# Kernel optimization log

Measured on AMD Instinct MI355X. Metric: run time of the kernel, lower is better.

Reference implementation:

```python
import jax, jax.numpy as jnp
import numpy as np

B, T, D, H = 2, 2048, 1024, 16
HD = D // H


def setup_inputs() -> dict:
    key = jax.random.key(0)
    ks = jax.random.split(key, 9)
    s = 1.0 / np.sqrt(D)
    return {
        "x": jax.random.normal(ks[0], (B, T, D), dtype=jnp.float32),
        "Wq": jax.random.normal(ks[1], (D, D), dtype=jnp.float32) * s,
        "bq": jnp.zeros((D,), dtype=jnp.float32),
        "Wk": jax.random.normal(ks[2], (D, D), dtype=jnp.float32) * s,
        "bk": jnp.zeros((D,), dtype=jnp.float32),
        "Wv": jax.random.normal(ks[3], (D, D), dtype=jnp.float32) * s,
        "bv": jnp.zeros((D,), dtype=jnp.float32),
        "Wo": jax.random.normal(ks[4], (D, D), dtype=jnp.float32) * s,
        "bo": jnp.zeros((D,), dtype=jnp.float32),
    }


def reference(x, Wq, bq, Wk, bk, Wv, bv, Wo, bo):
    b, t, d = x.shape
    # projections, split heads: (b, h, t, hd)
    def heads(y):
        return y.reshape(b, t, H, HD).transpose(0, 2, 1, 3)
    Q = heads(x @ Wq + bq)
    K = heads(x @ Wk + bk)
    V = heads(x @ Wv + bv)
    # scores scaled by sqrt(d) (full embed dim, faithful to source)
    score = jnp.einsum("bhid,bhjd->bhij", Q, K) / jnp.sqrt(jnp.float32(d))
    causal = jnp.triu(jnp.ones((t, t), dtype=bool), k=1)  # (t, t)
    score = jnp.where(causal, jnp.float32(-1e10), score)
    # FAITHFUL quirk: softmax over the HEAD axis (torch dim=1 of [b,h,t,t])
    weight = jax.nn.softmax(score, axis=1)
    out = jnp.einsum("bhij,bhjd->bhid", weight, V)
    out = out.transpose(0, 2, 1, 3).reshape(b, t, d)
    return out @ Wo + bo
```

## Files before the change

### kernel.cpp

```cpp
#include <hip/hip_runtime.h>
#include <hip/hip_bf16.h>

#define B_ 2
#define T_ 2048
#define D_ 1024
#define H_ 16

typedef __attribute__((ext_vector_type(8))) short bf16x8;
typedef __attribute__((ext_vector_type(4))) short bf16x4;
typedef __attribute__((ext_vector_type(4))) float f32x4;

__device__ __forceinline__ unsigned pack_bf16(float x, float y) {
  unsigned xb = __float_as_uint(x), yb = __float_as_uint(y);
  xb += 0x7fffu + ((xb >> 16) & 1u);
  yb += 0x7fffu + ((yb >> 16) & 1u);
  return (xb >> 16) | (yb & 0xffff0000u);
}
__device__ __forceinline__ unsigned short f2b(float x) {
  unsigned u = __float_as_uint(x);
  u += 0x7fffu + ((u >> 16) & 1u);
  return (unsigned short)(u >> 16);
}
__device__ __forceinline__ float blo(unsigned u) { return __uint_as_float(u << 16); }
__device__ __forceinline__ float bhi(unsigned u) { return __uint_as_float(u & 0xffff0000u); }

__device__ __forceinline__ void gld_lds16(const unsigned short* g, unsigned short* l) {
  __builtin_amdgcn_global_load_lds(
      (const __attribute__((address_space(1))) unsigned int*)g,
      (__attribute__((address_space(3))) unsigned int*)l, 16, 0, 0);
}

__global__ __launch_bounds__(256) void wtrans(const float* __restrict__ W0, const float* __restrict__ W1,
                                              const float* __restrict__ W2, const float* __restrict__ W3,
                                              unsigned short* __restrict__ T0, unsigned short* __restrict__ T1,
                                              unsigned short* __restrict__ T2, unsigned short* __restrict__ T3) {
  const int z = blockIdx.z;
  const float* W = z == 0 ? W0 : z == 1 ? W1 : z == 2 ? W2 : W3;
  unsigned short* T = z == 0 ? T0 : z == 1 ? T1 : z == 2 ? T2 : T3;
  __shared__ unsigned short t[64][72];
  const int k0 = blockIdx.x << 6, n0 = blockIdx.y << 6;
  const int r = threadIdx.x >> 2, c16 = (threadIdx.x & 3) << 4;
#pragma unroll
  for (int e = 0; e < 4; ++e) {
    const float4 v = *(const float4*)&W[(size_t)(k0 + r) * 1024 + n0 + c16 + e * 4];
    t[r][c16 + e * 4 + 0] = f2b(v.x);
    t[r][c16 + e * 4 + 1] = f2b(v.y);
    t[r][c16 + e * 4 + 2] = f2b(v.z);
    t[r][c16 + e * 4 + 3] = f2b(v.w);
  }
  __syncthreads();
  unsigned short o[16];
#pragma unroll
  for (int e = 0; e < 16; ++e) o[e] = t[c16 + e][r];
  unsigned short* dst = &T[(size_t)(n0 + r) * 1024 + k0 + c16];
  *(uint4*)&dst[0] = *(uint4*)&o[0];
  *(uint4*)&dst[8] = *(uint4*)&o[8];
}

__global__ __launch_bounds__(256) void xconv(const float* __restrict__ x, unsigned short* __restrict__ xb) {
  const int i = (blockIdx.x * 256 + threadIdx.x) * 8;
  const float4 a = *(const float4*)&x[i];
  const float4 b = *(const float4*)&x[i + 4];
  uint4 o;
  o.x = pack_bf16(a.x, a.y);
  o.y = pack_bf16(a.z, a.w);
  o.z = pack_bf16(b.x, b.y);
  o.w = pack_bf16(b.z, b.w);
  *(uint4*)&xb[i] = o;
}

template <bool BF16OUT>
__global__ __launch_bounds__(256) void gemm_mfma(const unsigned short* __restrict__ A,
                                                 const unsigned short* __restrict__ B0,
                                                 const unsigned short* __restrict__ B1,
                                                 const unsigned short* __restrict__ B2,
                                                 const float* __restrict__ bi0, const float* __restrict__ bi1,
                                                 const float* __restrict__ bi2,
                                                 void* __restrict__ Y0, void* __restrict__ Y1,
                                                 void* __restrict__ Y2) {
  const int z = blockIdx.z;
  const unsigned short* Bt = z == 0 ? B0 : z == 1 ? B1 : B2;
  const float* bias = z == 0 ? bi0 : z == 1 ? bi1 : bi2;
  void* Y = z == 0 ? Y0 : z == 1 ? Y1 : Y2;
  __shared__ unsigned short As[8192];
  __shared__ unsigned short Bs[8192];
  const int tid = threadIdx.x;
  const int m0 = blockIdx.y << 7, n0 = blockIdx.x << 7;
  const int w = tid >> 6, l = tid & 63, g = l >> 4, c = l & 15;
  const int wm = (w >> 1) << 6, wn = (w & 1) << 6;
  const int srow = tid >> 3;
  const int skel = ((tid & 7) ^ (srow & 7)) << 3;
  const unsigned short* ga = &A[(size_t)(m0 + srow) * 1024 + skel];
  const unsigned short* gb = &Bt[(size_t)(n0 + srow) * 1024 + skel];
  unsigned short* la = &As[tid << 3];
  unsigned short* lb = &Bs[tid << 3];
  f32x4 acc[4][4];
#pragma unroll
  for (int i = 0; i < 4; ++i)
#pragma unroll
    for (int j = 0; j < 4; ++j) acc[i][j] = {0.f, 0.f, 0.f, 0.f};
  for (int k0 = 0; k0 < 1024; k0 += 64) {
    __syncthreads();
#pragma unroll
    for (int a = 0; a < 4; ++a) {
      gld_lds16(ga + (size_t)(a << 5) * 1024 + k0, la + (a << 11));
      gld_lds16(gb + (size_t)(a << 5) * 1024 + k0, lb + (a << 11));
    }
    __syncthreads();
#pragma unroll
    for (int kc = 0; kc < 2; ++kc) {
      bf16x8 af[4], bfr[4];
#pragma unroll
      for (int mf = 0; mf < 4; ++mf) {
        const int m = wm + (mf << 4) + c;
        af[mf] = *(const bf16x8*)&As[((m << 6) + (kc << 5) + (g << 3)) ^ ((m & 7) << 3)];
      }
#pragma unroll
      for (int nf = 0; nf < 4; ++nf) {
        const int n = wn + (nf << 4) + c;
        bfr[nf] = *(const bf16x8*)&Bs[((n << 6) + (kc << 5) + (g << 3)) ^ ((n & 7) << 3)];
      }
#pragma unroll
      for (int mf = 0; mf < 4; ++mf)
#pragma unroll
        for (int nf = 0; nf < 4; ++nf)
          acc[mf][nf] = __builtin_amdgcn_mfma_f32_16x16x32_bf16(af[mf], bfr[nf], acc[mf][nf], 0, 0, 0);
    }
  }
#pragma unroll
  for (int nf = 0; nf < 4; ++nf) {
    const int n = n0 + wn + (nf << 4) + c;
    const float bb = bias[n];
#pragma unroll
    for (int mf = 0; mf < 4; ++mf) {
      const int mrow = m0 + wm + (mf << 4) + (g << 2);
#pragma unroll
      for (int r = 0; r < 4; ++r) {
        const float val = acc[mf][nf][r] + bb;
        if (BF16OUT)
          ((unsigned short*)Y)[((size_t)(mrow + r) << 10) + n] = f2b(val);
        else
          ((float*)Y)[((size_t)(mrow + r) << 10) + n] = val;
      }
    }
  }
}

__global__ __launch_bounds__(256) void transpose_bf16(const unsigned short* __restrict__ Vb,
                                                      unsigned short* __restrict__ Vt) {
  __shared__ unsigned short tile[64][73];
  const int b = blockIdx.z;
  const int t0 = blockIdx.x << 6, d0 = blockIdx.y << 6;
  const int row = threadIdx.x >> 2, cq = (threadIdx.x & 3) << 4;
  const unsigned short* src = &Vb[((size_t)((b << 11) + t0 + row) << 10) + d0 + cq];
  const uint4 va = *(const uint4*)&src[0];
  const uint4 vb2 = *(const uint4*)&src[8];
  const unsigned in[8] = {va.x, va.y, va.z, va.w, vb2.x, vb2.y, vb2.z, vb2.w};
#pragma unroll
  for (int e = 0; e < 8; ++e) {
    tile[row][cq + 2 * e] = (unsigned short)in[e];
    tile[row][cq + 2 * e + 1] = (unsigned short)(in[e] >> 16);
  }
  __syncthreads();
  unsigned o[8];
#pragma unroll
  for (int e = 0; e < 8; ++e)
    o[e] = (unsigned)tile[cq + 2 * e][row] | ((unsigned)tile[cq + 2 * e + 1][row] << 16);
  unsigned short* dst = &Vt[((size_t)((b << 10) + d0 + row) << 11) + t0 + cq];
  uint4 lo, hi;
  lo.x = o[0]; lo.y = o[1]; lo.z = o[2]; lo.w = o[3];
  hi.x = o[4]; hi.y = o[5]; hi.z = o[6]; hi.w = o[7];
  *(uint4*)&dst[0] = lo;
  *(uint4*)&dst[8] = hi;
}

__global__ __launch_bounds__(256) void vblk32(const unsigned short* __restrict__ Vb,
                                              float* __restrict__ Blk) {
  const int b = blockIdx.x >> 6, t = blockIdx.x & 63;
  const int d4 = threadIdx.x << 2;
  float s0 = 0.f, s1 = 0.f, s2 = 0.f, s3 = 0.f;
  for (int j = 0; j < 32; ++j) {
    const uint2 v = *(const uint2*)&Vb[((size_t)((b << 11) + (t << 5) + j) << 10) + d4];
    s0 += blo(v.x); s1 += bhi(v.x); s2 += blo(v.y); s3 += bhi(v.y);
  }
  float4 o = {s0, s1, s2, s3};
  *(float4*)&Blk[((size_t)((b << 6) + t) << 10) + d4] = o;
}

__global__ __launch_bounds__(256) void vsuffix32(const float* __restrict__ Blk, float* __restrict__ Suf) {
  const int idx = blockIdx.x * 256 + threadIdx.x;
  const int b = idx >> 10, d = idx & 1023;
  float s = 0.f;
  Suf[((size_t)(b * 65 + 64) << 10) + d] = 0.f;
  for (int t = 63; t >= 0; --t) {
    s += Blk[((size_t)((b << 6) + t) << 10) + d];
    Suf[((size_t)(b * 65 + t) << 10) + d] = s;
  }
}

__global__ __launch_bounds__(1024, 4) void attn_v16(const unsigned short* __restrict__ Qb,
                                                    const unsigned short* __restrict__ Kb,
                                                    const unsigned short* __restrict__ Vt,
                                                    unsigned short* __restrict__ P0,
                                                    unsigned short* __restrict__ P1,
                                                    unsigned short* __restrict__ P2,
                                                    unsigned short* __restrict__ P3) {
  __shared__ unsigned short Ks[2][16 * 1024];
  __shared__ unsigned short Vs[2][1024 * 16];
  __shared__ f32x4 Sx[2][8][64];

  const int combo = blockIdx.x;
  const int b = combo & 1, s = combo >> 1;
  const int qy = 63 - blockIdx.y;
  const int tid = threadIdx.x;
  const int w = tid >> 6, l = tid & 63, g = l >> 4, c = l & 15;
  const int isub = w >> 3, hp = w & 7;
  const float SC = 0.04508422f;
  unsigned short* AOp = s == 0 ? P0 : s == 1 ? P1 : s == 2 ? P2 : P3;

  const int krow0 = tid >> 7, kc8 = tid & 127;
  const int kscc = kc8 ^ (krow0 & 7);
  const int krow1 = (tid + 1024) >> 7, kc8b = tid & 127;
  const int ksccb = kc8b ^ (krow1 & 7);

#pragma unroll
  for (int ph = 0; ph < 2; ++ph) {
    const int q = ph ? (63 - qy) : qy;
    const int nt16 = (q + 1) << 1;
    const int i0w = (q << 5) + (isub << 4);
    const int ib = i0w + c;

    const unsigned short* qbase =
        &Qb[((size_t)((b << 11) + i0w + c) << 10) + (hp << 7) + (g << 3)];
    bf16x8 qf[4];
    qf[0] = *(const bf16x8*)&qbase[0];
    qf[1] = *(const bf16x8*)&qbase[32];
    qf[2] = *(const bf16x8*)&qbase[64];
    qf[3] = *(const bf16x8*)&qbase[96];

    f32x4 acc[2][4];
#pragma unroll
    for (int hh = 0; hh < 2; ++hh)
#pragma unroll
      for (int cc = 0; cc < 4; ++cc) acc[hh][cc] = {0.f, 0.f, 0.f, 0.f};

#pragma unroll
    for (int e = 0; e < 2; ++e) {
      const int eh = e ? (7 - s) : s;
      const int lo = eh << 4;
      const int hi = (lo + 16) < nt16 ? (lo + 16) : nt16;
      if (lo >= hi) continue;

      {
        const int j0e = lo << 4;
        gld_lds16(&Kb[((size_t)((b << 11) + j0e + krow0) << 10) + (kscc << 3)], &Ks[0][tid << 3]);
        gld_lds16(&Kb[((size_t)((b << 11) + j0e + krow1) << 10) + (ksccb << 3)],
                  &Ks[0][(tid + 1024) << 3]);
#pragma unroll
        for (int kk = 0; kk < 2; ++kk) {
          const int qq = tid + (kk << 10);
          const int d = qq >> 1, jc = qq & 1;
          const int joff = ((jc << 1) ^ (((d >> 2) & 1) << 1)) << 2;
          gld_lds16(&Vt[(((size_t)((b << 10) + d)) << 11) + j0e + joff], &Vs[0][qq << 3]);
        }
      }
      __syncthreads();

      for (int ts = lo; ts < hi; ++ts) {
        const int cur = (ts - lo) & 1;
        if (ts + 1 < hi) {
          const int j0e = (ts + 1) << 4;
          gld_lds16(&Kb[((size_t)((b << 11) + j0e + krow0) << 10) + (kscc << 3)],
                    &Ks[cur ^ 1][tid << 3]);
          gld_lds16(&Kb[((size_t)((b << 11) + j0e + krow1) << 10) + (ksccb << 3)],
                    &Ks[cur ^ 1][(tid + 1024) << 3]);
#pragma unroll
          for (int kk = 0; kk < 2; ++kk) {
            const int qq = tid + (kk << 10);
            const int d = qq >> 1, jc = qq & 1;
            const int joff = ((jc << 1) ^ (((d >> 2) & 1) << 1)) << 2;
            gld_lds16(&Vt[(((size_t)((b << 10) + d)) << 11) + j0e + joff],
                      &Vs[cur ^ 1][qq << 3]);
          }
        }
        const int j0 = ts << 4;
        const int kx = c & 7;
        f32x4 ex[2];
        f32x4 ps = {0.f, 0.f, 0.f, 0.f};
#pragma unroll
        for (int hh = 0; hh < 2; ++hh) {
          const int hc = ((hp << 1) + hh) << 3;
          const bf16x8 k0 = *(const bf16x8*)&Ks[cur][((c << 7) + ((hc + g) ^ kx)) << 3];
          const bf16x8 k1 = *(const bf16x8*)&Ks[cur][((c << 7) + ((hc + 4 + g) ^ kx)) << 3];
          f32x4 a = {0.f, 0.f, 0.f, 0.f};
          a = __builtin_amdgcn_mfma_f32_16x16x32_bf16(k0, qf[2 * hh], a, 0, 0, 0);
          a = __builtin_amdgcn_mfma_f32_16x16x32_bf16(k1, qf[2 * hh + 1], a, 0, 0, 0);
#pragma unroll
          for (int r = 0; r < 4; ++r) ex[hh][r] = exp2f(a[r] * SC);
          ps += ex[hh];
        }
        Sx[isub][hp][l] = ps;
        __syncthreads();
        f32x4 sum = Sx[isub][0][l];
#pragma unroll
        for (int d8 = 1; d8 < 8; ++d8) sum += Sx[isub][d8][l];
        f32x4 inv;
#pragma unroll
        for (int r = 0; r < 4; ++r) inv[r] = __builtin_amdgcn_rcpf(sum[r]);
        float wv[2][4];
        if (j0 + 15 <= i0w) {
#pragma unroll
          for (int hh = 0; hh < 2; ++hh)
#pragma unroll
            for (int r = 0; r < 4; ++r) wv[hh][r] = ex[hh][r] * inv[r];
        } else {
          const int jb = j0 + (g << 2);
#pragma unroll
          for (int hh = 0; hh < 2; ++hh)
#pragma unroll
            for (int r = 0; r < 4; ++r)
              wv[hh][r] = (jb + r > ib) ? 0.0625f : ex[hh][r] * inv[r];
        }
#pragma unroll
        for (int hh = 0; hh < 2; ++hh) {
          union { bf16x4 v; unsigned u[2]; } pa;
          pa.u[0] = pack_bf16(wv[hh][0], wv[hh][1]);
          pa.u[1] = pack_bf16(wv[hh][2], wv[hh][3]);
#pragma unroll
          for (int cc = 0; cc < 4; ++cc) {
            const int d = (((hp << 1) + hh) << 6) + (cc << 4) + c;
            const int up = g ^ (((d >> 2) & 1) << 1);
            union { bf16x4 v; unsigned u[2]; } vf;
            *(uint2*)&vf = *(const uint2*)&Vs[cur][(d << 4) + (up << 2)];
            acc[hh][cc] =
                __builtin_amdgcn_mfma_f32_16x16x16bf16_1k(pa.v, vf.v, acc[hh][cc], 0, 0, 0);
          }
        }
        __syncthreads();
      }
    }
#pragma unroll
    for (int hh = 0; hh < 2; ++hh)
#pragma unroll
      for (int cc = 0; cc < 4; ++cc) {
        const int d = (((hp << 1) + hh) << 6) + (cc << 4) + c;
#pragma unroll
        for (int r = 0; r < 4; ++r)
          AOp[((size_t)((b << 11) + i0w + (g << 2) + r) << 10) + d] = f2b(acc[hh][cc][r]);
      }
  }
}

__global__ __launch_bounds__(256) void aocvt(const unsigned short* __restrict__ P0,
                                             const unsigned short* __restrict__ P1,
                                             const unsigned short* __restrict__ P2,
                                             const unsigned short* __restrict__ P3,
                                             const float* __restrict__ Suf,
                                             unsigned short* __restrict__ AOb) {
  const int i = (blockIdx.x * 256 + threadIdx.x) << 3;
  const int m = i >> 10;
  const int b = m >> 11;
  const int sufidx = ((m & 2047) >> 5) + 1;
  const int d0 = i & 1023;
  const float* sp = &Suf[((size_t)(b * 65 + sufidx) << 10) + d0];
  const uint4 v0 = *(const uint4*)&P0[i];
  const uint4 v1 = *(const uint4*)&P1[i];
  const uint4 v2 = *(const uint4*)&P2[i];
  const uint4 v3 = *(const uint4*)&P3[i];
  const float4 s0 = *(const float4*)&sp[0];
  const float4 s1 = *(const float4*)&sp[4];
  uint4 o;
  o.x = pack_bf16(blo(v0.x) + blo(v1.x) + blo(v2.x) + blo(v3.x) + 0.0625f * s0.x,
                  bhi(v0.x) + bhi(v1.x) + bhi(v2.x) + bhi(v3.x) + 0.0625f * s0.y);
  o.y = pack_bf16(blo(v0.y) + blo(v1.y) + blo(v2.y) + blo(v3.y) + 0.0625f * s0.z,
                  bhi(v0.y) + bhi(v1.y) + bhi(v2.y) + bhi(v3.y) + 0.0625f * s0.w);
  o.z = pack_bf16(blo(v0.z) + blo(v1.z) + blo(v2.z) + blo(v3.z) + 0.0625f * s1.x,
                  bhi(v0.z) + bhi(v1.z) + bhi(v2.z) + bhi(v3.z) + 0.0625f * s1.y);
  o.w = pack_bf16(blo(v0.w) + blo(v1.w) + blo(v2.w) + blo(v3.w) + 0.0625f * s1.z,
                  bhi(v0.w) + bhi(v1.w) + bhi(v2.w) + bhi(v3.w) + 0.0625f * s1.w);
  *(uint4*)&AOb[i] = o;
}

extern "C" void kernel_launch(void* const* d_in, const int* in_sizes, int n_in,
                              void* d_out, int out_size, void* d_ws, size_t ws_size,
                              hipStream_t stream) {
  (void)in_sizes; (void)n_in; (void)out_size; (void)ws_size;
  const float* x = (const float*)d_in[0];
  const float* Wq = (const float*)d_in[1];
  const float* bq = (const float*)d_in[2];
  const float* Wk = (const float*)d_in[3];
  const float* bk = (const float*)d_in[4];
  const float* Wv = (const float*)d_in[5];
  const float* bv = (const float*)d_in[6];
  const float* Wo = (const float*)d_in[7];
  const float* bo = (const float*)d_in[8];
  float* out = (float*)d_out;
  char* ws = (char*)d_ws;

  const size_t MB = 1024 * 1024;
  unsigned short* xb  = (unsigned short*)(ws);
  unsigned short* Qb  = (unsigned short*)(ws + 8 * MB);
  unsigned short* Kb  = (unsigned short*)(ws + 16 * MB);
  unsigned short* Vb  = (unsigned short*)(ws + 24 * MB);
  unsigned short* Vt  = (unsigned short*)(ws + 32 * MB);
  unsigned short* Wqt = (unsigned short*)(ws + 40 * MB);
  unsigned short* Wkt = (unsigned short*)(ws + 42 * MB);
  unsigned short* Wvt = (unsigned short*)(ws + 44 * MB);
  unsigned short* Wot = (unsigned short*)(ws + 46 * MB);
  unsigned short* AOP2 = (unsigned short*)(ws + 48 * MB);
  unsigned short* AOP3 = (unsigned short*)(ws + 56 * MB);
  float* Blk = (float*)(ws + 40 * MB);
  float* Suf = (float*)(ws + 40 * MB + 512 * 1024);
  unsigned short* AOP0 = xb;
  unsigned short* AOP1 = Vb;
  unsigned short* AOb = Qb;

  hipLaunchKernelGGL(wtrans, dim3(16, 16, 4), dim3(256), 0, stream,
                     Wq, Wk, Wv, Wo, Wqt, Wkt, Wvt, Wot);
  hipLaunchKernelGGL(xconv, dim3(2048), dim3(256), 0, stream, x, xb);
  hipLaunchKernelGGL((gemm_mfma<true>), dim3(8, 32, 3), dim3(256), 0, stream,
                     xb, Wqt, Wkt, Wvt, bq, bk, bv, (void*)Qb, (void*)Kb, (void*)Vb);
  hipLaunchKernelGGL(transpose_bf16, dim3(32, 16, 2), dim3(256), 0, stream, Vb, Vt);
  hipLaunchKernelGGL(vblk32, dim3(128), dim3(256), 0, stream, Vb, Blk);
  hipLaunchKernelGGL(vsuffix32, dim3(8), dim3(256), 0, stream, Blk, Suf);
  hipLaunchKernelGGL(attn_v16, dim3(8, 32), dim3(1024), 0, stream,
                     Qb, Kb, Vt, AOP0, AOP1, AOP2, AOP3);
  hipLaunchKernelGGL(aocvt, dim3(2048), dim3(256), 0, stream,
                     AOP0, AOP1, AOP2, AOP3, Suf, AOb);
  hipLaunchKernelGGL((gemm_mfma<false>), dim3(8, 32, 1), dim3(256), 0, stream,
                     AOb, Wot, Wot, Wot, bo, bo, bo, (void*)out, (void*)out, (void*)out);
}
```

Measured before the change: 194.0 us.

## Fuse V projection with transpose and simplify attention tile address math

Adds a dedicated GEMM for the V projection that transposes through shared memory and writes Vt directly. This removes the separate Vb buffer and the transpose kernel, and the block-sum kernel now reads Vt. Inside the attention kernel, the K and V load pointers are precomputed once, and the cross-wave softmax partial sums are exchanged in LDS as bf16 rather than fp32. That halves the LDS traffic for the exchange but lowers the precision of the denominator.

```diff
diff --git a/kernel.cpp b/kernel.cpp
--- a/kernel.cpp
+++ b/kernel.cpp
@@ -146,45 +146,97 @@
   }
 }
 
-__global__ __launch_bounds__(256) void transpose_bf16(const unsigned short* __restrict__ Vb,
-                                                      unsigned short* __restrict__ Vt) {
-  __shared__ unsigned short tile[64][73];
-  const int b = blockIdx.z;
-  const int t0 = blockIdx.x << 6, d0 = blockIdx.y << 6;
-  const int row = threadIdx.x >> 2, cq = (threadIdx.x & 3) << 4;
-  const unsigned short* src = &Vb[((size_t)((b << 11) + t0 + row) << 10) + d0 + cq];
-  const uint4 va = *(const uint4*)&src[0];
-  const uint4 vb2 = *(const uint4*)&src[8];
-  const unsigned in[8] = {va.x, va.y, va.z, va.w, vb2.x, vb2.y, vb2.z, vb2.w};
-#pragma unroll
-  for (int e = 0; e < 8; ++e) {
-    tile[row][cq + 2 * e] = (unsigned short)in[e];
-    tile[row][cq + 2 * e + 1] = (unsigned short)(in[e] >> 16);
+__global__ __launch_bounds__(256) void gemm_vt(const unsigned short* __restrict__ A,
+                                               const unsigned short* __restrict__ Bt,
+                                               const float* __restrict__ bias,
+                                               unsigned short* __restrict__ Vt) {
+  __shared__ unsigned short As[8192];
+  __shared__ unsigned short Bs[8192];
+  __shared__ unsigned short sm[128][136];
+  const int tid = threadIdx.x;
+  const int m0 = blockIdx.y << 7, n0 = blockIdx.x << 7;
+  const int w = tid >> 6, l = tid & 63, g = l >> 4, c = l & 15;
+  const int wm = (w >> 1) << 6, wn = (w & 1) << 6;
+  const int srow = tid >> 3;
+  const int skel = ((tid & 7) ^ (srow & 7)) << 3;
+  const unsigned short* ga = &A[(size_t)(m0 + srow) * 1024 + skel];
+  const unsigned short* gb = &Bt[(size_t)(n0 + srow) * 1024 + skel];
+  unsigned short* la = &As[tid << 3];
+  unsigned short* lb = &Bs[tid << 3];
+  f32x4 acc[4][4];
+#pragma unroll
+  for (int i = 0; i < 4; ++i)
+#pragma unroll
+    for (int j = 0; j < 4; ++j) acc[i][j] = {0.f, 0.f, 0.f, 0.f};
+  for (int k0 = 0; k0 < 1024; k0 += 64) {
+    __syncthreads();
+#pragma unroll
+    for (int a = 0; a < 4; ++a) {
+      gld_lds16(ga + (size_t)(a << 5) * 1024 + k0, la + (a << 11));
+      gld_lds16(gb + (size_t)(a << 5) * 1024 + k0, lb + (a << 11));
+    }
+    __syncthreads();
+#pragma unroll
+    for (int kc = 0; kc < 2; ++kc) {
+      bf16x8 af[4], bfr[4];
+#pragma unroll
+      for (int mf = 0; mf < 4; ++mf) {
+        const int m = wm + (mf << 4) + c;
+        af[mf] = *(const bf16x8*)&As[((m << 6) + (kc << 5) + (g << 3)) ^ ((m & 7) << 3)];
+      }
+#pragma unroll
+      for (int nf = 0; nf < 4; ++nf) {
+        const int n = wn + (nf << 4) + c;
+        bfr[nf] = *(const bf16x8*)&Bs[((n << 6) + (kc << 5) + (g << 3)) ^ ((n & 7) << 3)];
+      }
+#pragma unroll
+      for (int mf = 0; mf < 4; ++mf)
+#pragma unroll
+        for (int nf = 0; nf < 4; ++nf)
+          acc[mf][nf] = __builtin_amdgcn_mfma_f32_16x16x32_bf16(af[mf], bfr[nf], acc[mf][nf], 0, 0, 0);
+    }
   }
   __syncthreads();
-  unsigned o[8];
-#pragma unroll
-  for (int e = 0; e < 8; ++e)
-    o[e] = (unsigned)tile[cq + 2 * e][row] | ((unsigned)tile[cq + 2 * e + 1][row] << 16);
-  unsigned short* dst = &Vt[((size_t)((b << 10) + d0 + row) << 11) + t0 + cq];
-  uint4 lo, hi;
-  lo.x = o[0]; lo.y = o[1]; lo.z = o[2]; lo.w = o[3];
-  hi.x = o[4]; hi.y = o[5]; hi.z = o[6]; hi.w = o[7];
-  *(uint4*)&dst[0] = lo;
-  *(uint4*)&dst[8] = hi;
-}
-
-__global__ __launch_bounds__(256) void vblk32(const unsigned short* __restrict__ Vb,
-                                              float* __restrict__ Blk) {
+#pragma unroll
+  for (int nf = 0; nf < 4; ++nf) {
+    const int nl = wn + (nf << 4) + c;
+    const float bb = bias[n0 + nl];
+#pragma unroll
+    for (int mf = 0; mf < 4; ++mf) {
+      const int ml = wm + (mf << 4) + (g << 2);
+      uint2 o;
+      o.x = pack_bf16(acc[mf][nf][0] + bb, acc[mf][nf][1] + bb);
+      o.y = pack_bf16(acc[mf][nf][2] + bb, acc[mf][nf][3] + bb);
+      *(uint2*)&sm[nl][ml] = o;
+    }
+  }
+  __syncthreads();
+  const int bb2 = m0 >> 11, mr0 = m0 & 2047;
+#pragma unroll
+  for (int it = 0; it < 8; ++it) {
+    const int u = tid + (it << 8);
+    const int ns = u >> 4, mc = (u & 15) << 3;
+    *(uint4*)&Vt[(((size_t)((bb2 << 10) + n0 + ns)) << 11) + mr0 + mc] = *(const uint4*)&sm[ns][mc];
+  }
+}
+
+__global__ __launch_bounds__(256) void vblk32t(const unsigned short* __restrict__ Vt,
+                                               float* __restrict__ Blk) {
   const int b = blockIdx.x >> 6, t = blockIdx.x & 63;
-  const int d4 = threadIdx.x << 2;
-  float s0 = 0.f, s1 = 0.f, s2 = 0.f, s3 = 0.f;
-  for (int j = 0; j < 32; ++j) {
-    const uint2 v = *(const uint2*)&Vb[((size_t)((b << 11) + (t << 5) + j) << 10) + d4];
-    s0 += blo(v.x); s1 += bhi(v.x); s2 += blo(v.y); s3 += bhi(v.y);
-  }
-  float4 o = {s0, s1, s2, s3};
-  *(float4*)&Blk[((size_t)((b << 6) + t) << 10) + d4] = o;
+#pragma unroll
+  for (int dd = 0; dd < 4; ++dd) {
+    const int d = threadIdx.x + (dd << 8);
+    const unsigned short* vr = &Vt[(((size_t)((b << 10) + d)) << 11) + (t << 5)];
+    float s = 0.f;
+#pragma unroll
+    for (int qq = 0; qq < 4; ++qq) {
+      const uint2 v0 = *(const uint2*)&vr[qq << 3];
+      const uint2 v1 = *(const uint2*)&vr[(qq << 3) + 4];
+      s += blo(v0.x) + bhi(v0.x) + blo(v0.y) + bhi(v0.y);
+      s += blo(v1.x) + bhi(v1.x) + blo(v1.y) + bhi(v1.y);
+    }
+    Blk[(((size_t)((b << 6) + t)) << 10) + d] = s;
+  }
 }
 
 __global__ __launch_bounds__(256) void vsuffix32(const float* __restrict__ Blk, float* __restrict__ Suf) {
@@ -198,7 +250,7 @@
   }
 }
 
-__global__ __launch_bounds__(1024, 4) void attn_v16(const unsigned short* __restrict__ Qb,
+__global__ __launch_bounds__(1024, 4) void attn_v17(const unsigned short* __restrict__ Qb,
                                                     const unsigned short* __restrict__ Kb,
                                                     const unsigned short* __restrict__ Vt,
                                                     unsigned short* __restrict__ P0,
@@ -207,7 +259,7 @@
                                                     unsigned short* __restrict__ P3) {
   __shared__ unsigned short Ks[2][16 * 1024];
   __shared__ unsigned short Vs[2][1024 * 16];
-  __shared__ f32x4 Sx[2][8][64];
+  __shared__ uint2 Sx[2][8][64];
 
   const int combo = blockIdx.x;
   const int b = combo & 1, s = combo >> 1;
@@ -219,9 +271,17 @@
   unsigned short* AOp = s == 0 ? P0 : s == 1 ? P1 : s == 2 ? P2 : P3;
 
   const int krow0 = tid >> 7, kc8 = tid & 127;
-  const int kscc = kc8 ^ (krow0 & 7);
-  const int krow1 = (tid + 1024) >> 7, kc8b = tid & 127;
-  const int ksccb = kc8b ^ (krow1 & 7);
+  const int kscc0 = kc8 ^ (krow0 & 7);
+  const int krow1 = krow0 + 8;
+  const int kscc1 = kc8 ^ (krow1 & 7);
+  const unsigned short* kp0 = &Kb[(((size_t)((b << 11) + krow0)) << 10) + (kscc0 << 3)];
+  const unsigned short* kp1 = &Kb[(((size_t)((b << 11) + krow1)) << 10) + (kscc1 << 3)];
+  const int vd0 = tid >> 1, vjc = tid & 1;
+  const int vjo0 = ((vjc << 1) ^ (((vd0 >> 2) & 1) << 1)) << 2;
+  const int vd1 = vd0 + 512;
+  const int vjo1 = ((vjc << 1) ^ (((vd1 >> 2) & 1) << 1)) << 2;
+  const unsigned short* vp0 = &Vt[(((size_t)((b << 10) + vd0)) << 11) + vjo0];
+  const unsigned short* vp1 = &Vt[(((size_t)((b << 10) + vd1)) << 11) + vjo1];
 
 #pragma unroll
   for (int ph = 0; ph < 2; ++ph) {
@@ -252,36 +312,24 @@
       if (lo >= hi) continue;
 
       {
-        const int j0e = lo << 4;
-        gld_lds16(&Kb[((size_t)((b << 11) + j0e + krow0) << 10) + (kscc << 3)], &Ks[0][tid << 3]);
-        gld_lds16(&Kb[((size_t)((b << 11) + j0e + krow1) << 10) + (ksccb << 3)],
-                  &Ks[0][(tid + 1024) << 3]);
-#pragma unroll
-        for (int kk = 0; kk < 2; ++kk) {
-          const int qq = tid + (kk << 10);
-          const int d = qq >> 1, jc = qq & 1;
-          const int joff = ((jc << 1) ^ (((d >> 2) & 1) << 1)) << 2;
-          gld_lds16(&Vt[(((size_t)((b << 10) + d)) << 11) + j0e + joff], &Vs[0][qq << 3]);
-        }
+        const size_t ko = ((size_t)lo << 14);
+        gld_lds16(kp0 + ko, &Ks[0][tid << 3]);
+        gld_lds16(kp1 + ko, &Ks[0][(tid + 1024) << 3]);
+        const int jo = lo << 4;
+        gld_lds16(vp0 + jo, &Vs[0][tid << 3]);
+        gld_lds16(vp1 + jo, &Vs[0][(tid + 1024) << 3]);
       }
       __syncthreads();
 
       for (int ts = lo; ts < hi; ++ts) {
         const int cur = (ts - lo) & 1;
         if (ts + 1 < hi) {
-          const int j0e = (ts + 1) << 4;
-          gld_lds16(&Kb[((size_t)((b << 11) + j0e + krow0) << 10) + (kscc << 3)],
-                    &Ks[cur ^ 1][tid << 3]);
-          gld_lds16(&Kb[((size_t)((b << 11) + j0e + krow1) << 10) + (ksccb << 3)],
-                    &Ks[cur ^ 1][(tid + 1024) << 3]);
-#pragma unroll
-          for (int kk = 0; kk < 2; ++kk) {
-            const int qq = tid + (kk << 10);
-            const int d = qq >> 1, jc = qq & 1;
-            const int joff = ((jc << 1) ^ (((d >> 2) & 1) << 1)) << 2;
-            gld_lds16(&Vt[(((size_t)((b << 10) + d)) << 11) + j0e + joff],
-                      &Vs[cur ^ 1][qq << 3]);
-          }
+          const size_t ko = ((size_t)(ts + 1) << 14);
+          gld_lds16(kp0 + ko, &Ks[cur ^ 1][tid << 3]);
+          gld_lds16(kp1 + ko, &Ks[cur ^ 1][(tid + 1024) << 3]);
+          const int jo = (ts + 1) << 4;
+          gld_lds16(vp0 + jo, &Vs[cur ^ 1][tid << 3]);
+          gld_lds16(vp1 + jo, &Vs[cur ^ 1][(tid + 1024) << 3]);
         }
         const int j0 = ts << 4;
         const int kx = c & 7;
@@ -299,11 +347,20 @@
           for (int r = 0; r < 4; ++r) ex[hh][r] = exp2f(a[r] * SC);
           ps += ex[hh];
         }
-        Sx[isub][hp][l] = ps;
+        uint2 pp;
+        pp.x = pack_bf16(ps[0], ps[1]);
+        pp.y = pack_bf16(ps[2], ps[3]);
+        Sx[isub][hp][l] = pp;
         __syncthreads();
-        f32x4 sum = Sx[isub][0][l];
-#pragma unroll
-        for (int d8 = 1; d8 < 8; ++d8) sum += Sx[isub][d8][l];
+        f32x4 sum = {0.f, 0.f, 0.f, 0.f};
+#pragma unroll
+        for (int d8 = 0; d8 < 8; ++d8) {
+          const uint2 u = Sx[isub][d8][l];
+          sum[0] += blo(u.x);
+          sum[1] += bhi(u.x);
+          sum[2] += blo(u.y);
+          sum[3] += bhi(u.y);
+        }
         f32x4 inv;
 #pragma unroll
         for (int r = 0; r < 4; ++r) inv[r] = __builtin_amdgcn_rcpf(sum[r]);
@@ -401,7 +458,7 @@
   unsigned short* xb  = (unsigned short*)(ws);
   unsigned short* Qb  = (unsigned short*)(ws + 8 * MB);
   unsigned short* Kb  = (unsigned short*)(ws + 16 * MB);
-  unsigned short* Vb  = (unsigned short*)(ws + 24 * MB);
+  unsigned short* AOP1 = (unsigned short*)(ws + 24 * MB);
   unsigned short* Vt  = (unsigned short*)(ws + 32 * MB);
   unsigned short* Wqt = (unsigned short*)(ws + 40 * MB);
   unsigned short* Wkt = (unsigned short*)(ws + 42 * MB);
@@ -412,18 +469,17 @@
   float* Blk = (float*)(ws + 40 * MB);
   float* Suf = (float*)(ws + 40 * MB + 512 * 1024);
   unsigned short* AOP0 = xb;
-  unsigned short* AOP1 = Vb;
   unsigned short* AOb = Qb;
 
   hipLaunchKernelGGL(wtrans, dim3(16, 16, 4), dim3(256), 0, stream,
                      Wq, Wk, Wv, Wo, Wqt, Wkt, Wvt, Wot);
   hipLaunchKernelGGL(xconv, dim3(2048), dim3(256), 0, stream, x, xb);
-  hipLaunchKernelGGL((gemm_mfma<true>), dim3(8, 32, 3), dim3(256), 0, stream,
-                     xb, Wqt, Wkt, Wvt, bq, bk, bv, (void*)Qb, (void*)Kb, (void*)Vb);
-  hipLaunchKernelGGL(transpose_bf16, dim3(32, 16, 2), dim3(256), 0, stream, Vb, Vt);
-  hipLaunchKernelGGL(vblk32, dim3(128), dim3(256), 0, stream, Vb, Blk);
+  hipLaunchKernelGGL((gemm_mfma<true>), dim3(8, 32, 2), dim3(256), 0, stream,
+                     xb, Wqt, Wkt, Wkt, bq, bk, bk, (void*)Qb, (void*)Kb, (void*)Kb);
+  hipLaunchKernelGGL(gemm_vt, dim3(8, 32), dim3(256), 0, stream, xb, Wvt, bv, Vt);
+  hipLaunchKernelGGL(vblk32t, dim3(128), dim3(256), 0, stream, Vt, Blk);
   hipLaunchKernelGGL(vsuffix32, dim3(8), dim3(256), 0, stream, Blk, Suf);
-  hipLaunchKernelGGL(attn_v16, dim3(8, 32), dim3(1024), 0, stream,
+  hipLaunchKernelGGL(attn_v17, dim3(8, 32), dim3(1024), 0, stream,
                      Qb, Kb, Vt, AOP0, AOP1, AOP2, AOP3);
   hipLaunchKernelGGL(aocvt, dim3(2048), dim3(256), 0, stream,
                      AOP0, AOP1, AOP2, AOP3, Suf, AOb);
```

Result: no change. 196.0 us (+1.0%).
